# Kernel tuning notes

Hardware: AMD Instinct MI355X
Metric: run time of the kernel (lower is better)

## Reference

```python
import jax, jax.numpy as jnp
import numpy as np

B_, S, H, Dh, N = 2, 2048, 8, 64, 32

def setup_inputs() -> dict:
    key = jax.random.key(0)
    k = jax.random.split(key, 6)
    return {
        'u':  jax.random.normal(k[0], (B_, S, H, Dh), dtype=jnp.float32),
        'dt': jax.random.uniform(k[1], (B_, S, H, Dh), dtype=jnp.float32),
        'A':  jax.random.uniform(k[2], (H, Dh, N), dtype=jnp.float32),
        'B':  jax.random.normal(k[3], (B_, S, H, N), dtype=jnp.float32),
        'C':  jax.random.normal(k[4], (B_, S, H, N), dtype=jnp.float32),
        'D':  jax.random.normal(k[5], (H,), dtype=jnp.float32),
    }

def reference(u, dt, A, B, C, D):
    # Selective SSM scan (Mamba-style):
    #   h_t = dA_t * h_{t-1} + dB_t * u_t ; y_t = <h_t, C_t> + D * u_t
    dt_e = dt[..., None]                              # [b,s,h,d,1]
    dA = jnp.exp(-dt_e * A)                           # [b,s,h,d,n]
    Bu = (dt_e * B[:, :, :, None, :]) * u[..., None]  # [b,s,h,d,n]

    def combine(x, y):
        a1, b1 = x
        a2, b2 = y
        return a1 * a2, a2 * b1 + b2

    _, h = jax.lax.associative_scan(combine, (dA, Bu), axis=1)  # inclusive scan over seq
    out = jnp.sum(h * C[:, :, :, None, :], axis=-1)             # [b,s,h,d]
    out = out + D[None, None, :, None] * u
    return out
```

## Files before the change

### kernel.cpp

```cpp
#include <hip/hip_runtime.h>

namespace {

constexpr int S_LEN = 2048;
constexpr int H_N   = 8;
constexpr int D_DIM = 64;
constexpr int N_DIM = 32;
constexpr int TW    = 16;
constexpr int NKC   = S_LEN / TW;
constexpr int SEGL  = NKC / 4;
constexpr float NLOG2E = -1.4426950408889634f;


__global__ __launch_bounds__(256, 4) void ssm_k1(
    const float* __restrict__ dtp, const float* __restrict__ up,
    const float* __restrict__ Ap,  const float* __restrict__ Bp,
    float* __restrict__ sdtb, float* __restrict__ bagg)
{
    __shared__ float lB[4][TW * 32];

    const int tid  = threadIdx.x;
    const int w    = tid >> 6;
    const int lane = tid & 63;
    const int pp   = w >> 1;
    const int dh   = w & 1;
    const int dlow = lane & 31;
    const int nh   = lane >> 5;
    const int bh   = blockIdx.x >> 6;
    const int kcg  = blockIdx.x & 63;
    const int kc   = kcg * 2 + pp;
    const int b = bh >> 3, hh = bh & 7;
    const int d  = dh * 32 + dlow;
    const int n0 = nh * 16;
    const int ch = bh * 64 + d;
    const int s0 = kc * TW;

    const int base_ud = b * (S_LEN * 512) + hh * 64 + d;
    const int bB      = b * (S_LEN * 256) + hh * 32 + s0 * 256;

#pragma unroll
    for (int it = 0; it < 2; ++it) {
        const int idx = it * 64 + lane;
        const int row = idx >> 3, col = idx & 7;
        const float4 v = *(const float4*)(Bp + bB + row * 256 + col * 4);
        *(float4*)&lB[w][idx * 4] = v;
    }

    float dtv[TW], uv[TW];
#pragma unroll
    for (int t = 0; t < TW; ++t) {
        dtv[t] = dtp[base_ud + (s0 + t) * 512];
        uv[t]  = up [base_ud + (s0 + t) * 512];
    }

    float Aneg[16];
    {
        const float* Arow = Ap + (hh * D_DIM + d) * N_DIM + n0;
#pragma unroll
        for (int j = 0; j < 4; ++j) {
            float4 a4 = *(const float4*)(Arow + j * 4);
            Aneg[4*j+0] = NLOG2E * a4.x; Aneg[4*j+1] = NLOG2E * a4.y;
            Aneg[4*j+2] = NLOG2E * a4.z; Aneg[4*j+3] = NLOG2E * a4.w;
        }
    }

    float bA[16];
#pragma unroll
    for (int j = 0; j < 16; ++j) bA[j] = 0.0f;
    float sdt = 0.0f;

#pragma unroll 4
    for (int t = 0; t < TW; ++t) {
        const float kk = dtv[t] * uv[t];
        sdt += dtv[t];
#pragma unroll
        for (int j = 0; j < 4; ++j) {
            const float4 Bv = *(const float4*)&lB[w][t * 32 + n0 + j * 4];
#pragma unroll
            for (int q = 0; q < 4; ++q) {
                const int jn = j * 4 + q;
                const float bq = (q == 0) ? Bv.x : (q == 1) ? Bv.y : (q == 2) ? Bv.z : Bv.w;
                const float e = __builtin_amdgcn_exp2f(dtv[t] * Aneg[jn]);
                bA[jn] = fmaf(e, bA[jn], kk * bq);
            }
        }
    }

    if (nh == 0) sdtb[kc * 1024 + ch] = sdt;
    {
        float* dst = bagg + (size_t)kc * 32768 + ch * 32 + n0;
#pragma unroll
        for (int j = 0; j < 4; ++j)
            *(float4*)(dst + j * 4) = make_float4(bA[4*j+0], bA[4*j+1], bA[4*j+2], bA[4*j+3]);
    }
}

__global__ __launch_bounds__(256) void ssm_k2(
    const float* __restrict__ sdtb, const float* __restrict__ bagg,
    const float* __restrict__ Ap,   float* __restrict__ pref)
{
    const int T   = blockIdx.x * 256 + threadIdx.x;
    const int seg = T & 3;
    const int n   = (T >> 2) & 31;
    const int ch  = T >> 7;
    const int d   = ch & 63;
    const int hh  = (ch >> 6) & 7;
    const float Aneg1 = NLOG2E * Ap[(hh * D_DIM + d) * N_DIM + n];

    const int k0 = seg * SEGL;
    const size_t base = (size_t)ch * 32 + n;

    float bb[SEGL], av[SEGL];
#pragma unroll
    for (int i = 0; i < SEGL; ++i) {
        bb[i] = bagg[(size_t)(k0 + i) * 32768 + base];
        av[i] = sdtb[(k0 + i) * 1024 + ch];
    }
#pragma unroll
    for (int i = 0; i < SEGL; ++i)
        av[i] = __builtin_amdgcn_exp2f(Aneg1 * av[i]);

    float bseg = 0.0f, Aseg = 1.0f;
#pragma unroll
    for (int i = 0; i < SEGL; ++i) {
        bseg = fmaf(av[i], bseg, bb[i]);
        Aseg *= av[i];
    }

    {
        float Au = __shfl_up(Aseg, 1, 4), bu = __shfl_up(bseg, 1, 4);
        if (seg >= 1) { bseg = fmaf(Aseg, bu, bseg); Aseg *= Au; }
        Au = __shfl_up(Aseg, 2, 4); bu = __shfl_up(bseg, 2, 4);
        if (seg >= 2) { bseg = fmaf(Aseg, bu, bseg); Aseg *= Au; }
    }
    const float ebu = __shfl_up(bseg, 1, 4);
    float p = (seg == 0) ? 0.0f : ebu;

#pragma unroll
    for (int i = 0; i < SEGL; ++i) {
        pref[(size_t)(k0 + i) * 32768 + base] = p;
        p = fmaf(av[i], p, bb[i]);
    }
}

__global__ __launch_bounds__(256, 4) void ssm_k3(
    const float* __restrict__ dtp, const float* __restrict__ up,
    const float* __restrict__ Ap,  const float* __restrict__ Bp,
    const float* __restrict__ Cp,  const float* __restrict__ Dp,
    const float* __restrict__ pref, float* __restrict__ outp)
{
    __shared__ float lB[4][TW * 32];
    __shared__ float lC[4][TW * 32];

    const int tid  = threadIdx.x;
    const int w    = tid >> 6;
    const int lane = tid & 63;
    const int pp   = w >> 1;
    const int dh   = w & 1;
    const int dlow = lane & 31;
    const int nh   = lane >> 5;
    const int bh   = blockIdx.x >> 6;
    const int kcg  = blockIdx.x & 63;
    const int kc   = kcg * 2 + pp;
    const int b = bh >> 3, hh = bh & 7;
    const int d  = dh * 32 + dlow;
    const int n0 = nh * 16;
    const int ch = bh * 64 + d;
    const int s0 = kc * TW;

    const int base_ud = b * (S_LEN * 512) + hh * 64 + d;
    const int bB      = b * (S_LEN * 256) + hh * 32 + s0 * 256;

    float h[16];
    {
        const float* ps = pref + (size_t)kc * 32768 + ch * 32 + n0;
#pragma unroll
        for (int j = 0; j < 4; ++j) {
            float4 v = *(const float4*)(ps + j * 4);
            h[4*j+0] = v.x; h[4*j+1] = v.y; h[4*j+2] = v.z; h[4*j+3] = v.w;
        }
    }

#pragma unroll
    for (int it = 0; it < 2; ++it) {
        const int idx = it * 64 + lane;
        const int row = idx >> 3, col = idx & 7;
        const float4 vb = *(const float4*)(Bp + bB + row * 256 + col * 4);
        const float4 vc = *(const float4*)(Cp + bB + row * 256 + col * 4);
        *(float4*)&lB[w][idx * 4] = vb;
        *(float4*)&lC[w][idx * 4] = vc;
    }

    float dtv[TW], uv[TW];
#pragma unroll
    for (int t = 0; t < TW; ++t) {
        dtv[t] = dtp[base_ud + (s0 + t) * 512];
        uv[t]  = up [base_ud + (s0 + t) * 512];
    }

    float Aneg[16];
    {
        const float* Arow = Ap + (hh * D_DIM + d) * N_DIM + n0;
#pragma unroll
        for (int j = 0; j < 4; ++j) {
            float4 a4 = *(const float4*)(Arow + j * 4);
            Aneg[4*j+0] = NLOG2E * a4.x; Aneg[4*j+1] = NLOG2E * a4.y;
            Aneg[4*j+2] = NLOG2E * a4.z; Aneg[4*j+3] = NLOG2E * a4.w;
        }
    }

    const float Dv = Dp[hh];

#pragma unroll 4
    for (int t = 0; t < TW; ++t) {
        const float kk = dtv[t] * uv[t];
        float y0 = 0.0f, y1 = 0.0f, y2 = 0.0f, y3 = 0.0f;
#pragma unroll
        for (int j = 0; j < 4; ++j) {
            const float4 Bv = *(const float4*)&lB[w][t * 32 + n0 + j * 4];
            const float4 Cv = *(const float4*)&lC[w][t * 32 + n0 + j * 4];
#pragma unroll
            for (int q = 0; q < 4; ++q) {
                const int jn = j * 4 + q;
                const float bq = (q == 0) ? Bv.x : (q == 1) ? Bv.y : (q == 2) ? Bv.z : Bv.w;
                const float cq = (q == 0) ? Cv.x : (q == 1) ? Cv.y : (q == 2) ? Cv.z : Cv.w;
                const float e = __builtin_amdgcn_exp2f(dtv[t] * Aneg[jn]);
                h[jn] = fmaf(e, h[jn], kk * bq);
                if (q == 0)      y0 = fmaf(h[jn], cq, y0);
                else if (q == 1) y1 = fmaf(h[jn], cq, y1);
                else if (q == 2) y2 = fmaf(h[jn], cq, y2);
                else             y3 = fmaf(h[jn], cq, y3);
            }
        }
        float y = (y0 + y1) + (y2 + y3);
        y += __shfl_xor(y, 32);
        if (nh == 0) outp[base_ud + (s0 + t) * 512] = fmaf(Dv, uv[t], y);
    }
}

}

extern "C" void kernel_launch(void* const* d_in, const int* in_sizes, int n_in,
                              void* d_out, int out_size, void* d_ws, size_t ws_size,
                              hipStream_t stream)
{
    const float* u  = (const float*)d_in[0];
    const float* dt = (const float*)d_in[1];
    const float* A  = (const float*)d_in[2];
    const float* B  = (const float*)d_in[3];
    const float* C  = (const float*)d_in[4];
    const float* D  = (const float*)d_in[5];
    float* out = (float*)d_out;

    float* sdtb = (float*)d_ws;
    float* bagg = sdtb + (size_t)NKC * 1024;
    float* pref = bagg + (size_t)NKC * 32 * 1024;

    ssm_k1<<<dim3(16 * 64), dim3(256), 0, stream>>>(dt, u, A, B, sdtb, bagg);
    ssm_k2<<<dim3(512),     dim3(256), 0, stream>>>(sdtb, bagg, A, pref);
    ssm_k3<<<dim3(16 * 64), dim3(256), 0, stream>>>(dt, u, A, B, C, D, pref, out);
}
```

Measured before the change: 47.28 us.

## Double scan chunk length and remap threads to 16 d × 4 state quarters

Chunk length goes from 16 to 32 timesteps, so there are half as many chunks. This halves the per-chunk aggregate and prefix buffers written and read between the three kernels, and shortens the middle prefix kernel's sequential segments. Each block now handles one chunk: each wave covers 16 d channels and each lane covers 8 of the 32 states, so the dt/u loads are split into two 16-step halves to limit register use. The costs are more redundant dt/u loads across lanes, a longer sequential loop per thread, and an extra cross-lane shuffle for the output reduction.

```diff
diff --git a/kernel.cpp b/kernel.cpp
--- a/kernel.cpp
+++ b/kernel.cpp
@@ -6,7 +6,7 @@
 constexpr int H_N   = 8;
 constexpr int D_DIM = 64;
 constexpr int N_DIM = 32;
-constexpr int TW    = 16;
+constexpr int TW    = 32;
 constexpr int NKC   = S_LEN / TW;
 constexpr int SEGL  = NKC / 4;
 constexpr float NLOG2E = -1.4426950408889634f;
@@ -22,16 +22,13 @@
     const int tid  = threadIdx.x;
     const int w    = tid >> 6;
     const int lane = tid & 63;
-    const int pp   = w >> 1;
-    const int dh   = w & 1;
-    const int dlow = lane & 31;
-    const int nh   = lane >> 5;
+    const int dl   = lane & 15;
+    const int nq   = lane >> 4;
     const int bh   = blockIdx.x >> 6;
-    const int kcg  = blockIdx.x & 63;
-    const int kc   = kcg * 2 + pp;
+    const int kc   = blockIdx.x & 63;
     const int b = bh >> 3, hh = bh & 7;
-    const int d  = dh * 32 + dlow;
-    const int n0 = nh * 16;
+    const int d  = w * 16 + dl;
+    const int n0 = nq * 8;
     const int ch = bh * 64 + d;
     const int s0 = kc * TW;
 
@@ -39,59 +36,62 @@
     const int bB      = b * (S_LEN * 256) + hh * 32 + s0 * 256;
 
 #pragma unroll
-    for (int it = 0; it < 2; ++it) {
+    for (int it = 0; it < 4; ++it) {
         const int idx = it * 64 + lane;
         const int row = idx >> 3, col = idx & 7;
         const float4 v = *(const float4*)(Bp + bB + row * 256 + col * 4);
         *(float4*)&lB[w][idx * 4] = v;
     }
 
-    float dtv[TW], uv[TW];
-#pragma unroll
-    for (int t = 0; t < TW; ++t) {
-        dtv[t] = dtp[base_ud + (s0 + t) * 512];
-        uv[t]  = up [base_ud + (s0 + t) * 512];
-    }
-
-    float Aneg[16];
+    float Aneg[8];
     {
         const float* Arow = Ap + (hh * D_DIM + d) * N_DIM + n0;
 #pragma unroll
-        for (int j = 0; j < 4; ++j) {
+        for (int j = 0; j < 2; ++j) {
             float4 a4 = *(const float4*)(Arow + j * 4);
             Aneg[4*j+0] = NLOG2E * a4.x; Aneg[4*j+1] = NLOG2E * a4.y;
             Aneg[4*j+2] = NLOG2E * a4.z; Aneg[4*j+3] = NLOG2E * a4.w;
         }
     }
 
-    float bA[16];
-#pragma unroll
-    for (int j = 0; j < 16; ++j) bA[j] = 0.0f;
+    float bA[8];
+#pragma unroll
+    for (int j = 0; j < 8; ++j) bA[j] = 0.0f;
     float sdt = 0.0f;
 
+#pragma unroll
+    for (int st = 0; st < 2; ++st) {
+        float dtv[16], uv[16];
+#pragma unroll
+        for (int t2 = 0; t2 < 16; ++t2) {
+            const int s = s0 + st * 16 + t2;
+            dtv[t2] = dtp[base_ud + s * 512];
+            uv[t2]  = up [base_ud + s * 512];
+        }
 #pragma unroll 4
-    for (int t = 0; t < TW; ++t) {
-        const float kk = dtv[t] * uv[t];
-        sdt += dtv[t];
-#pragma unroll
-        for (int j = 0; j < 4; ++j) {
-            const float4 Bv = *(const float4*)&lB[w][t * 32 + n0 + j * 4];
-#pragma unroll
-            for (int q = 0; q < 4; ++q) {
-                const int jn = j * 4 + q;
-                const float bq = (q == 0) ? Bv.x : (q == 1) ? Bv.y : (q == 2) ? Bv.z : Bv.w;
-                const float e = __builtin_amdgcn_exp2f(dtv[t] * Aneg[jn]);
-                bA[jn] = fmaf(e, bA[jn], kk * bq);
+        for (int t2 = 0; t2 < 16; ++t2) {
+            const int tt = st * 16 + t2;
+            const float kk = dtv[t2] * uv[t2];
+            sdt += dtv[t2];
+#pragma unroll
+            for (int j = 0; j < 2; ++j) {
+                const float4 Bv = *(const float4*)&lB[w][tt * 32 + n0 + j * 4];
+#pragma unroll
+                for (int q = 0; q < 4; ++q) {
+                    const int jn = j * 4 + q;
+                    const float bq = (q == 0) ? Bv.x : (q == 1) ? Bv.y : (q == 2) ? Bv.z : Bv.w;
+                    const float e = __builtin_amdgcn_exp2f(dtv[t2] * Aneg[jn]);
+                    bA[jn] = fmaf(e, bA[jn], kk * bq);
+                }
             }
         }
     }
 
-    if (nh == 0) sdtb[kc * 1024 + ch] = sdt;
+    if (nq == 0) sdtb[kc * 1024 + ch] = sdt;
     {
         float* dst = bagg + (size_t)kc * 32768 + ch * 32 + n0;
-#pragma unroll
-        for (int j = 0; j < 4; ++j)
-            *(float4*)(dst + j * 4) = make_float4(bA[4*j+0], bA[4*j+1], bA[4*j+2], bA[4*j+3]);
+        *(float4*)(dst + 0) = make_float4(bA[0], bA[1], bA[2], bA[3]);
+        *(float4*)(dst + 4) = make_float4(bA[4], bA[5], bA[6], bA[7]);
     }
 }
 
@@ -155,34 +155,30 @@
     const int tid  = threadIdx.x;
     const int w    = tid >> 6;
     const int lane = tid & 63;
-    const int pp   = w >> 1;
-    const int dh   = w & 1;
-    const int dlow = lane & 31;
-    const int nh   = lane >> 5;
+    const int dl   = lane & 15;
+    const int nq   = lane >> 4;
     const int bh   = blockIdx.x >> 6;
-    const int kcg  = blockIdx.x & 63;
-    const int kc   = kcg * 2 + pp;
+    const int kc   = blockIdx.x & 63;
     const int b = bh >> 3, hh = bh & 7;
-    const int d  = dh * 32 + dlow;
-    const int n0 = nh * 16;
+    const int d  = w * 16 + dl;
+    const int n0 = nq * 8;
     const int ch = bh * 64 + d;
     const int s0 = kc * TW;
 
     const int base_ud = b * (S_LEN * 512) + hh * 64 + d;
     const int bB      = b * (S_LEN * 256) + hh * 32 + s0 * 256;
 
-    float h[16];
+    float h[8];
     {
         const float* ps = pref + (size_t)kc * 32768 + ch * 32 + n0;
-#pragma unroll
-        for (int j = 0; j < 4; ++j) {
-            float4 v = *(const float4*)(ps + j * 4);
-            h[4*j+0] = v.x; h[4*j+1] = v.y; h[4*j+2] = v.z; h[4*j+3] = v.w;
-        }
-    }
-
-#pragma unroll
-    for (int it = 0; it < 2; ++it) {
+        float4 v0 = *(const float4*)(ps + 0);
+        float4 v1 = *(const float4*)(ps + 4);
+        h[0] = v0.x; h[1] = v0.y; h[2] = v0.z; h[3] = v0.w;
+        h[4] = v1.x; h[5] = v1.y; h[6] = v1.z; h[7] = v1.w;
+    }
+
+#pragma unroll
+    for (int it = 0; it < 4; ++it) {
         const int idx = it * 64 + lane;
         const int row = idx >> 3, col = idx & 7;
         const float4 vb = *(const float4*)(Bp + bB + row * 256 + col * 4);
@@ -191,18 +187,11 @@
         *(float4*)&lC[w][idx * 4] = vc;
     }
 
-    float dtv[TW], uv[TW];
-#pragma unroll
-    for (int t = 0; t < TW; ++t) {
-        dtv[t] = dtp[base_ud + (s0 + t) * 512];
-        uv[t]  = up [base_ud + (s0 + t) * 512];
-    }
-
-    float Aneg[16];
+    float Aneg[8];
     {
         const float* Arow = Ap + (hh * D_DIM + d) * N_DIM + n0;
 #pragma unroll
-        for (int j = 0; j < 4; ++j) {
+        for (int j = 0; j < 2; ++j) {
             float4 a4 = *(const float4*)(Arow + j * 4);
             Aneg[4*j+0] = NLOG2E * a4.x; Aneg[4*j+1] = NLOG2E * a4.y;
             Aneg[4*j+2] = NLOG2E * a4.z; Aneg[4*j+3] = NLOG2E * a4.w;
@@ -211,30 +200,42 @@
 
     const float Dv = Dp[hh];
 
+#pragma unroll
+    for (int st = 0; st < 2; ++st) {
+        float dtv[16], uv[16];
+#pragma unroll
+        for (int t2 = 0; t2 < 16; ++t2) {
+            const int s = s0 + st * 16 + t2;
+            dtv[t2] = dtp[base_ud + s * 512];
+            uv[t2]  = up [base_ud + s * 512];
+        }
 #pragma unroll 4
-    for (int t = 0; t < TW; ++t) {
-        const float kk = dtv[t] * uv[t];
-        float y0 = 0.0f, y1 = 0.0f, y2 = 0.0f, y3 = 0.0f;
-#pragma unroll
-        for (int j = 0; j < 4; ++j) {
-            const float4 Bv = *(const float4*)&lB[w][t * 32 + n0 + j * 4];
-            const float4 Cv = *(const float4*)&lC[w][t * 32 + n0 + j * 4];
-#pragma unroll
-            for (int q = 0; q < 4; ++q) {
-                const int jn = j * 4 + q;
-                const float bq = (q == 0) ? Bv.x : (q == 1) ? Bv.y : (q == 2) ? Bv.z : Bv.w;
-                const float cq = (q == 0) ? Cv.x : (q == 1) ? Cv.y : (q == 2) ? Cv.z : Cv.w;
-                const float e = __builtin_amdgcn_exp2f(dtv[t] * Aneg[jn]);
-                h[jn] = fmaf(e, h[jn], kk * bq);
-                if (q == 0)      y0 = fmaf(h[jn], cq, y0);
-                else if (q == 1) y1 = fmaf(h[jn], cq, y1);
-                else if (q == 2) y2 = fmaf(h[jn], cq, y2);
-                else             y3 = fmaf(h[jn], cq, y3);
+        for (int t2 = 0; t2 < 16; ++t2) {
+            const int tt = st * 16 + t2;
+            const float kk = dtv[t2] * uv[t2];
+            float y0 = 0.0f, y1 = 0.0f, y2 = 0.0f, y3 = 0.0f;
+#pragma unroll
+            for (int j = 0; j < 2; ++j) {
+                const float4 Bv = *(const float4*)&lB[w][tt * 32 + n0 + j * 4];
+                const float4 Cv = *(const float4*)&lC[w][tt * 32 + n0 + j * 4];
+#pragma unroll
+                for (int q = 0; q < 4; ++q) {
+                    const int jn = j * 4 + q;
+                    const float bq = (q == 0) ? Bv.x : (q == 1) ? Bv.y : (q == 2) ? Bv.z : Bv.w;
+                    const float cq = (q == 0) ? Cv.x : (q == 1) ? Cv.y : (q == 2) ? Cv.z : Cv.w;
+                    const float e = __builtin_amdgcn_exp2f(dtv[t2] * Aneg[jn]);
+                    h[jn] = fmaf(e, h[jn], kk * bq);
+                    if (q == 0)      y0 = fmaf(h[jn], cq, y0);
+                    else if (q == 1) y1 = fmaf(h[jn], cq, y1);
+                    else if (q == 2) y2 = fmaf(h[jn], cq, y2);
+                    else             y3 = fmaf(h[jn], cq, y3);
+                }
             }
-        }
-        float y = (y0 + y1) + (y2 + y3);
-        y += __shfl_xor(y, 32);
-        if (nh == 0) outp[base_ud + (s0 + t) * 512] = fmaf(Dv, uv[t], y);
+            float y = (y0 + y1) + (y2 + y3);
+            y += __shfl_xor(y, 16);
+            y += __shfl_xor(y, 32);
+            if (nq == 0) outp[base_ud + (s0 + tt) * 512] = fmaf(Dv, uv[t2], y);
+        }
     }
 }
 
@@ -256,7 +257,7 @@
     float* bagg = sdtb + (size_t)NKC * 1024;
     float* pref = bagg + (size_t)NKC * 32 * 1024;
 
-    ssm_k1<<<dim3(16 * 64), dim3(256), 0, stream>>>(dt, u, A, B, sdtb, bagg);
-    ssm_k2<<<dim3(512),     dim3(256), 0, stream>>>(sdtb, bagg, A, pref);
-    ssm_k3<<<dim3(16 * 64), dim3(256), 0, stream>>>(dt, u, A, B, C, D, pref, out);
-}
+    ssm_k1<<<dim3(16 * NKC), dim3(256), 0, stream>>>(dt, u, A, B, sdtb, bagg);
+    ssm_k2<<<dim3(512),      dim3(256), 0, stream>>>(sdtb, bagg, A, pref);
+    ssm_k3<<<dim3(16 * NKC), dim3(256), 0, stream>>>(dt, u, A, B, C, D, pref, out);
+}
```

Result: faster. 43.37 us (-8.3%).
